# Optimization experiments

Measured on AMD Instinct MI355X. Metric: run time of the kernel, lower is better.

Reference implementation:

```python
import jax, jax.numpy as jnp
import numpy as np

B, S, D, P, W = 16, 100, 8192, 100, 3  # batch, seq, feat dim, proj width, window size


def setup_inputs() -> dict:
    key = jax.random.key(0)
    ks = jax.random.split(key, 6)
    return {
        "x": jax.random.normal(ks[0], (B, S, D), dtype=jnp.float32),
        "wq": jax.random.normal(ks[1], (D, P), dtype=jnp.float32) * (1.0 / np.sqrt(D)),
        "wk": jax.random.normal(ks[2], (D, P), dtype=jnp.float32) * (1.0 / np.sqrt(D)),
        "wv": jax.random.normal(ks[3], (D, P), dtype=jnp.float32) * (1.0 / np.sqrt(D)),
        "forwardpad": jax.random.normal(ks[4], (B, 1, D), dtype=jnp.float32),
        "backwardpad": jax.random.normal(ks[5], (B, 1, D), dtype=jnp.float32),
    }


def reference(x, wq, wk, wv, forwardpad, backwardpad):
    # pad: (B, S+2, D)
    padded = jnp.concatenate([forwardpad, x, backwardpad], axis=1)
    # gather all 100 overlapping size-3 windows at once: (B, S, W, D)
    idx = jnp.arange(S)[:, None] + jnp.arange(W)[None, :]  # (S, W)
    windows = padded[:, idx, :]
    # shared projections across all windows (original recomputed per window)
    q = jnp.einsum("bswd,dp->bswp", windows, wq)
    k = jnp.einsum("bswd,dp->bswp", windows, wk)
    v = jnp.einsum("bswd,dp->bswp", windows, wv)
    # per-window 3x3 attention
    scores = jnp.einsum("bswp,bsup->bswu", q, k)  # (B, S, W, W)
    attn = jax.nn.softmax(scores, axis=-1)
    out = jnp.einsum("bswu,bsup->bswp", attn, v)  # (B, S, W, P)
    # original concatenates windows along seq then takes [:, 1::3, :] -> center token of each window
    return out[:, :, 1, :]  # (B, S, P)
```

## Files before the change

### kernel.cpp

```cpp
#include <hip/hip_runtime.h>
#include <hip/hip_bf16.h>

constexpr int Dk   = 8192;
constexpr int Bb   = 16;
constexpr int Ss   = 100;
constexpr int Pp   = 100;
constexpr int MROW = 1632;
constexpr int MPAD = 1664;
constexpr int NT   = 20;
constexpr int NCC  = 320;
constexpr int KG   = 1024;
constexpr int KC   = 32;
constexpr int CH   = 5;

constexpr size_t B_SEG   = (size_t)NT * KG * 128;
constexpr size_t PSTRIDE = (size_t)MPAD * NCC;

typedef short s8v __attribute__((ext_vector_type(8)));
typedef short s4v __attribute__((ext_vector_type(4)));
typedef float f4v __attribute__((ext_vector_type(4)));

__device__ inline unsigned short f2bf_rne(float f) {
    unsigned u = __float_as_uint(f);
    u += 0x7fffu + ((u >> 16) & 1u);
    return (unsigned short)(u >> 16);
}

__global__ __launch_bounds__(256) void pack_b(
    const float* __restrict__ wq, const float* __restrict__ wk,
    const float* __restrict__ wv,
    short* __restrict__ b_hi, short* __restrict__ b_lo) {
    const int id = blockIdx.x * 256 + threadIdx.x;
    const int n  = id % NCC;
    const int kg = id / NCC;
    if (kg >= KG) return;

    const float* w = nullptr; int p = 0;
    if (n < 100)      { w = wq; p = n; }
    else if (n < 200) { w = wk; p = n - 100; }
    else if (n < 300) { w = wv; p = n - 200; }

    s8v hi, lo;
    #pragma unroll
    for (int j = 0; j < 8; ++j) {
        const float v = w ? w[(size_t)(kg * 8 + j) * Pp + p] : 0.0f;
        const unsigned u = __float_as_uint(v);
        hi[j] = (short)(unsigned short)(u >> 16);
        const float hf = __uint_as_float(u & 0xffff0000u);
        lo[j] = (short)f2bf_rne(v - hf);
    }
    const size_t doff = ((size_t)(n >> 4) * KG + kg) * 128 + (size_t)(n & 15) * 8;
    *(s8v*)(b_hi + doff) = hi;
    *(s8v*)(b_lo + doff) = lo;
}

__global__ __launch_bounds__(256) void qkv_fused(
    const float* __restrict__ x, const float* __restrict__ fpad,
    const float* __restrict__ bpad,
    const short* __restrict__ b_hi, const short* __restrict__ b_lo,
    unsigned short* __restrict__ part) {
    __shared__ __align__(16) short ahis[1024];
    __shared__ __align__(16) short alos[1024];

    const int mb   = blockIdx.x;
    const int kc   = blockIdx.y;
    const int tid  = threadIdx.x;
    const int w    = tid >> 6;
    const int l    = tid & 63;
    const int m    = l & 15;
    const int quad = l >> 4;

    const int sr  = tid >> 3;
    const int skq = tid & 7;
    const float* srow;
    {
        const int r = mb * 32 + sr;
        if (r >= MROW) srow = fpad;
        else {
            const int b = r / 102, rr = r - b * 102;
            if (rr == 0)        srow = fpad + (size_t)b * Dk;
            else if (rr == 101) srow = bpad + (size_t)b * Dk;
            else                srow = x + ((size_t)b * Ss + (rr - 1)) * Dk;
        }
    }
    const int woff = ((sr >> 4) * 4 + (skq >> 1)) * 128 + (sr & 15) * 8 + (skq & 1) * 4;

    f4v acc[2][5];
    #pragma unroll
    for (int i = 0; i < 2; ++i)
        #pragma unroll
        for (int j = 0; j < 5; ++j) {
            f4v z = {0.f, 0.f, 0.f, 0.f};
            acc[i][j] = z;
        }

    for (int s = 0; s < 8; ++s) {
        const float4 v = *(const float4*)(srow + kc * 256 + s * 32 + skq * 4);
        const float vv[4] = {v.x, v.y, v.z, v.w};
        s4v hi4, lo4;
        #pragma unroll
        for (int jj = 0; jj < 4; ++jj) {
            const unsigned u = __float_as_uint(vv[jj]);
            hi4[jj] = (short)(unsigned short)(u >> 16);
            const float hf = __uint_as_float(u & 0xffff0000u);
            lo4[jj] = (short)f2bf_rne(vv[jj] - hf);
        }
        __syncthreads();
        *(s4v*)&ahis[woff] = hi4;
        *(s4v*)&alos[woff] = lo4;
        __syncthreads();

        const s8v ah0 = *(const s8v*)&ahis[(quad * 16 + m) * 8];
        const s8v ah1 = *(const s8v*)&ahis[((4 + quad) * 16 + m) * 8];
        const s8v al0 = *(const s8v*)&alos[(quad * 16 + m) * 8];
        const s8v al1 = *(const s8v*)&alos[((4 + quad) * 16 + m) * 8];

        const int kgg = kc * 32 + s * 4 + quad;
        #pragma unroll
        for (int j = 0; j < 5; ++j) {
            const size_t bo = ((size_t)(w * 5 + j) * KG + kgg) * 128 + (size_t)m * 8;
            const s8v bh = *(const s8v*)(b_hi + bo);
            const s8v bl = *(const s8v*)(b_lo + bo);
            acc[0][j] = __builtin_amdgcn_mfma_f32_16x16x32_bf16(ah0, bh, acc[0][j], 0, 0, 0);
            acc[1][j] = __builtin_amdgcn_mfma_f32_16x16x32_bf16(ah1, bh, acc[1][j], 0, 0, 0);
            acc[0][j] = __builtin_amdgcn_mfma_f32_16x16x32_bf16(al0, bh, acc[0][j], 0, 0, 0);
            acc[1][j] = __builtin_amdgcn_mfma_f32_16x16x32_bf16(al1, bh, acc[1][j], 0, 0, 0);
            acc[0][j] = __builtin_amdgcn_mfma_f32_16x16x32_bf16(ah0, bl, acc[0][j], 0, 0, 0);
            acc[1][j] = __builtin_amdgcn_mfma_f32_16x16x32_bf16(ah1, bl, acc[1][j], 0, 0, 0);
        }
    }

    unsigned short* __restrict__ pout = part + (size_t)kc * PSTRIDE;
    #pragma unroll
    for (int i = 0; i < 2; ++i) {
        #pragma unroll
        for (int j = 0; j < 5; ++j) {
            const int col  = (w * 5 + j) * 16 + m;
            const int row0 = mb * 32 + i * 16 + quad * 4;
            #pragma unroll
            for (int r = 0; r < 4; ++r)
                pout[(size_t)(row0 + r) * NCC + col] = f2bf_rne(acc[i][j][r]);
        }
    }
}

__global__ __launch_bounds__(256) void attn3(
    const unsigned short* __restrict__ part, float* __restrict__ out) {
    const int blk = blockIdx.x;
    const int b  = blk / (Ss / CH);
    const int c  = blk % (Ss / CH);
    const int s0 = c * CH;
    const int tid = threadIdx.x;

    __shared__ float red[CH + 2][304];
    __shared__ float sc[CH][3];

    for (int idx = tid; idx < (CH + 2) * 300; idx += 256) {
        const int row = idx / 300, col = idx % 300;
        const size_t base = (size_t)(b * 102 + s0 + row) * NCC + col;
        float sum = 0.0f;
        #pragma unroll
        for (int k = 0; k < KC; ++k)
            sum += __uint_as_float((unsigned)part[(size_t)k * PSTRIDE + base] << 16);
        red[row][col] = sum;
    }
    __syncthreads();

    if (tid < CH * 3 * 16) {
        const int d = tid >> 4, g = tid & 15;
        const int ss = d / 3, u = d % 3;
        float ps = 0.0f;
        #pragma unroll
        for (int t = 0; t < 7; ++t) {
            const int p = g + t * 16;
            if (p < Pp) ps += red[ss + 1][p] * red[ss + u][100 + p];
        }
        #pragma unroll
        for (int off = 8; off > 0; off >>= 1) ps += __shfl_down(ps, off, 16);
        if (g == 0) sc[ss][u] = ps;
    }
    __syncthreads();

    for (int idx = tid; idx < CH * Pp; idx += 256) {
        const int ss = idx / Pp, p = idx % Pp;
        const float a0 = sc[ss][0], a1 = sc[ss][1], a2 = sc[ss][2];
        const float mx = fmaxf(a0, fmaxf(a1, a2));
        const float e0 = __expf(a0 - mx), e1 = __expf(a1 - mx), e2 = __expf(a2 - mx);
        const float inv = 1.0f / (e0 + e1 + e2);
        out[(size_t)(b * Ss + s0 + ss) * Pp + p] =
            inv * (e0 * red[ss][200 + p] + e1 * red[ss + 1][200 + p] +
                   e2 * red[ss + 2][200 + p]);
    }
}

extern "C" void kernel_launch(void* const* d_in, const int* in_sizes, int n_in,
                              void* d_out, int out_size, void* d_ws, size_t ws_size,
                              hipStream_t stream) {
    const float* x    = (const float*)d_in[0];
    const float* wq   = (const float*)d_in[1];
    const float* wk   = (const float*)d_in[2];
    const float* wv   = (const float*)d_in[3];
    const float* fpad = (const float*)d_in[4];
    const float* bpad = (const float*)d_in[5];
    float* out = (float*)d_out;

    short* b_hi = (short*)d_ws;
    short* b_lo = b_hi + B_SEG;
    unsigned short* part = (unsigned short*)(b_lo + B_SEG);

    pack_b<<<(NCC * KG) / 256, 256, 0, stream>>>(wq, wk, wv, b_hi, b_lo);
    qkv_fused<<<dim3(52, KC), 256, 0, stream>>>(x, fpad, bpad, b_hi, b_lo, part);
    attn3<<<Bb * (Ss / CH), 256, 0, stream>>>(part, out);
}
```

Before: 155.4 us.

## Double GEMM M-tile, fragment-native fp16 partials, and separate split-K reduce kernel

The QKV GEMM block now covers 64 rows instead of 32, so each B fragment load from global memory feeds four MFMA row tiles. This halves B-operand traffic and halves the number of M blocks. Partial sums are stored in fp16 in the MFMA fragment layout using vectorized 8-byte writes, and a new reduce kernel sums the 32 K-chunks with coalesced loads and writes an fp32 QKV matrix. The attention kernel then reads the reduced values directly. In exchange there is an extra kernel launch and workspace buffer, higher register pressure from 20 accumulators that may lower occupancy, and a possible fp16 range or precision risk in the partials.

After: 157.7 us. About the same (+1.5%).

```diff
diff --git a/kernel.cpp b/kernel.cpp
--- a/kernel.cpp
+++ b/kernel.cpp
@@ -1,20 +1,23 @@
 #include <hip/hip_runtime.h>
 #include <hip/hip_bf16.h>
+#include <hip/hip_fp16.h>
 
 constexpr int Dk   = 8192;
 constexpr int Bb   = 16;
 constexpr int Ss   = 100;
 constexpr int Pp   = 100;
 constexpr int MROW = 1632;
-constexpr int MPAD = 1664;
 constexpr int NT   = 20;
 constexpr int NCC  = 320;
+constexpr int NQ   = 304;
 constexpr int KG   = 1024;
 constexpr int KC   = 32;
 constexpr int CH   = 5;
+constexpr int MB   = 26;
+constexpr int GFR  = MB * 4 * 20;
 
 constexpr size_t B_SEG   = (size_t)NT * KG * 128;
-constexpr size_t PSTRIDE = (size_t)MPAD * NCC;
+constexpr size_t PSTRIDE = (size_t)GFR * 256;
 
 typedef short s8v __attribute__((ext_vector_type(8)));
 typedef short s4v __attribute__((ext_vector_type(4)));
@@ -59,8 +62,8 @@
     const float* __restrict__ bpad,
     const short* __restrict__ b_hi, const short* __restrict__ b_lo,
     unsigned short* __restrict__ part) {
-    __shared__ __align__(16) short ahis[1024];
-    __shared__ __align__(16) short alos[1024];
+    __shared__ __align__(16) short ahis[2048];
+    __shared__ __align__(16) short alos[2048];
 
     const int mb   = blockIdx.x;
     const int kc   = blockIdx.y;
@@ -70,50 +73,58 @@
     const int m    = l & 15;
     const int quad = l >> 4;
 
-    const int sr  = tid >> 3;
-    const int skq = tid & 7;
-    const float* srow;
+    const int srow = tid >> 2;
+    const int skq  = tid & 3;
+    const float* sp;
     {
-        const int r = mb * 32 + sr;
-        if (r >= MROW) srow = fpad;
+        const int r = mb * 64 + srow;
+        if (r >= MROW) sp = fpad;
         else {
             const int b = r / 102, rr = r - b * 102;
-            if (rr == 0)        srow = fpad + (size_t)b * Dk;
-            else if (rr == 101) srow = bpad + (size_t)b * Dk;
-            else                srow = x + ((size_t)b * Ss + (rr - 1)) * Dk;
-        }
-    }
-    const int woff = ((sr >> 4) * 4 + (skq >> 1)) * 128 + (sr & 15) * 8 + (skq & 1) * 4;
-
-    f4v acc[2][5];
-    #pragma unroll
-    for (int i = 0; i < 2; ++i)
+            if (rr == 0)        sp = fpad + (size_t)b * Dk;
+            else if (rr == 101) sp = bpad + (size_t)b * Dk;
+            else                sp = x + ((size_t)b * Ss + (rr - 1)) * Dk;
+        }
+        sp += kc * 256 + skq * 4;
+    }
+    const int w0 = (((srow >> 4) * 4 + (skq >> 1)) * 16 + (srow & 15)) * 8 + (skq & 1) * 4;
+    const int w1 = (((srow >> 4) * 4 + 2 + (skq >> 1)) * 16 + (srow & 15)) * 8 + (skq & 1) * 4;
+
+    f4v acc[4][5];
+    #pragma unroll
+    for (int i = 0; i < 4; ++i)
         #pragma unroll
         for (int j = 0; j < 5; ++j) {
             f4v z = {0.f, 0.f, 0.f, 0.f};
             acc[i][j] = z;
         }
 
+    #pragma unroll
     for (int s = 0; s < 8; ++s) {
-        const float4 v = *(const float4*)(srow + kc * 256 + s * 32 + skq * 4);
-        const float vv[4] = {v.x, v.y, v.z, v.w};
-        s4v hi4, lo4;
+        const float4 va = *(const float4*)(sp + s * 32);
+        const float4 vb = *(const float4*)(sp + s * 32 + 16);
+        const float vv[8] = {va.x, va.y, va.z, va.w, vb.x, vb.y, vb.z, vb.w};
+        s4v h0, l0, h1, l1;
         #pragma unroll
         for (int jj = 0; jj < 4; ++jj) {
-            const unsigned u = __float_as_uint(vv[jj]);
-            hi4[jj] = (short)(unsigned short)(u >> 16);
-            const float hf = __uint_as_float(u & 0xffff0000u);
-            lo4[jj] = (short)f2bf_rne(vv[jj] - hf);
+            unsigned u = __float_as_uint(vv[jj]);
+            h0[jj] = (short)(unsigned short)(u >> 16);
+            l0[jj] = (short)f2bf_rne(vv[jj] - __uint_as_float(u & 0xffff0000u));
+            u = __float_as_uint(vv[4 + jj]);
+            h1[jj] = (short)(unsigned short)(u >> 16);
+            l1[jj] = (short)f2bf_rne(vv[4 + jj] - __uint_as_float(u & 0xffff0000u));
         }
         __syncthreads();
-        *(s4v*)&ahis[woff] = hi4;
-        *(s4v*)&alos[woff] = lo4;
+        *(s4v*)&ahis[w0] = h0;  *(s4v*)&alos[w0] = l0;
+        *(s4v*)&ahis[w1] = h1;  *(s4v*)&alos[w1] = l1;
         __syncthreads();
 
-        const s8v ah0 = *(const s8v*)&ahis[(quad * 16 + m) * 8];
-        const s8v ah1 = *(const s8v*)&ahis[((4 + quad) * 16 + m) * 8];
-        const s8v al0 = *(const s8v*)&alos[(quad * 16 + m) * 8];
-        const s8v al1 = *(const s8v*)&alos[((4 + quad) * 16 + m) * 8];
+        s8v ah[4], al[4];
+        #pragma unroll
+        for (int i = 0; i < 4; ++i) {
+            ah[i] = *(const s8v*)&ahis[((i * 4 + quad) * 16 + m) * 8];
+            al[i] = *(const s8v*)&alos[((i * 4 + quad) * 16 + m) * 8];
+        }
 
         const int kgg = kc * 32 + s * 4 + quad;
         #pragma unroll
@@ -121,31 +132,67 @@
             const size_t bo = ((size_t)(w * 5 + j) * KG + kgg) * 128 + (size_t)m * 8;
             const s8v bh = *(const s8v*)(b_hi + bo);
             const s8v bl = *(const s8v*)(b_lo + bo);
-            acc[0][j] = __builtin_amdgcn_mfma_f32_16x16x32_bf16(ah0, bh, acc[0][j], 0, 0, 0);
-            acc[1][j] = __builtin_amdgcn_mfma_f32_16x16x32_bf16(ah1, bh, acc[1][j], 0, 0, 0);
-            acc[0][j] = __builtin_amdgcn_mfma_f32_16x16x32_bf16(al0, bh, acc[0][j], 0, 0, 0);
-            acc[1][j] = __builtin_amdgcn_mfma_f32_16x16x32_bf16(al1, bh, acc[1][j], 0, 0, 0);
-            acc[0][j] = __builtin_amdgcn_mfma_f32_16x16x32_bf16(ah0, bl, acc[0][j], 0, 0, 0);
-            acc[1][j] = __builtin_amdgcn_mfma_f32_16x16x32_bf16(ah1, bl, acc[1][j], 0, 0, 0);
-        }
-    }
-
-    unsigned short* __restrict__ pout = part + (size_t)kc * PSTRIDE;
-    #pragma unroll
-    for (int i = 0; i < 2; ++i) {
+            #pragma unroll
+            for (int i = 0; i < 4; ++i)
+                acc[i][j] = __builtin_amdgcn_mfma_f32_16x16x32_bf16(ah[i], bh, acc[i][j], 0, 0, 0);
+            #pragma unroll
+            for (int i = 0; i < 4; ++i)
+                acc[i][j] = __builtin_amdgcn_mfma_f32_16x16x32_bf16(al[i], bh, acc[i][j], 0, 0, 0);
+            #pragma unroll
+            for (int i = 0; i < 4; ++i)
+                acc[i][j] = __builtin_amdgcn_mfma_f32_16x16x32_bf16(ah[i], bl, acc[i][j], 0, 0, 0);
+        }
+    }
+
+    #pragma unroll
+    for (int i = 0; i < 4; ++i) {
         #pragma unroll
         for (int j = 0; j < 5; ++j) {
-            const int col  = (w * 5 + j) * 16 + m;
-            const int row0 = mb * 32 + i * 16 + quad * 4;
-            #pragma unroll
-            for (int r = 0; r < 4; ++r)
-                pout[(size_t)(row0 + r) * NCC + col] = f2bf_rne(acc[i][j][r]);
-        }
+            const int g = (mb * 4 + w) * 20 + i * 5 + j;
+            const size_t idx = (((size_t)kc * GFR + g) * 64 + l) * 4;
+            ushort4 u;
+            u.x = __half_as_ushort(__float2half(acc[i][j][0]));
+            u.y = __half_as_ushort(__float2half(acc[i][j][1]));
+            u.z = __half_as_ushort(__float2half(acc[i][j][2]));
+            u.w = __half_as_ushort(__float2half(acc[i][j][3]));
+            *(ushort4*)(part + idx) = u;
+        }
+    }
+}
+
+__global__ __launch_bounds__(256) void reduce_k(
+    const unsigned short* __restrict__ part, float* __restrict__ qkv) {
+    const int t = blockIdx.x * 256 + threadIdx.x;
+    const int g = t >> 6, l = t & 63;
+    const size_t base = ((size_t)g * 64 + l) * 4;
+
+    float s0 = 0.f, s1 = 0.f, s2 = 0.f, s3 = 0.f;
+    #pragma unroll
+    for (int k = 0; k < KC; ++k) {
+        const ushort4 u = *(const ushort4*)(part + base + (size_t)k * PSTRIDE);
+        s0 += __half2float(__ushort_as_half(u.x));
+        s1 += __half2float(__ushort_as_half(u.y));
+        s2 += __half2float(__ushort_as_half(u.z));
+        s3 += __half2float(__ushort_as_half(u.w));
+    }
+
+    const int mb = g / 80, rem = g - mb * 80;
+    const int nw = rem / 20, fi = rem - nw * 20;
+    const int i = fi / 5, j = fi - i * 5;
+    const int quad = l >> 4, m = l & 15;
+    const int row = mb * 64 + i * 16 + quad * 4;
+    const int col = (nw * 5 + j) * 16 + m;
+    if (col < NQ) {
+        float* q = qkv + (size_t)row * NQ + col;
+        q[0]      = s0;
+        q[NQ]     = s1;
+        q[2 * NQ] = s2;
+        q[3 * NQ] = s3;
     }
 }
 
 __global__ __launch_bounds__(256) void attn3(
-    const unsigned short* __restrict__ part, float* __restrict__ out) {
+    const float* __restrict__ qkv, float* __restrict__ out) {
     const int blk = blockIdx.x;
     const int b  = blk / (Ss / CH);
     const int c  = blk % (Ss / CH);
@@ -157,12 +204,7 @@
 
     for (int idx = tid; idx < (CH + 2) * 300; idx += 256) {
         const int row = idx / 300, col = idx % 300;
-        const size_t base = (size_t)(b * 102 + s0 + row) * NCC + col;
-        float sum = 0.0f;
-        #pragma unroll
-        for (int k = 0; k < KC; ++k)
-            sum += __uint_as_float((unsigned)part[(size_t)k * PSTRIDE + base] << 16);
-        red[row][col] = sum;
+        red[row][col] = qkv[(size_t)(b * 102 + s0 + row) * NQ + col];
     }
     __syncthreads();
 
@@ -207,8 +249,10 @@
     short* b_hi = (short*)d_ws;
     short* b_lo = b_hi + B_SEG;
     unsigned short* part = (unsigned short*)(b_lo + B_SEG);
+    float* qkv = (float*)(part + (size_t)KC * PSTRIDE);
 
     pack_b<<<(NCC * KG) / 256, 256, 0, stream>>>(wq, wk, wv, b_hi, b_lo);
-    qkv_fused<<<dim3(52, KC), 256, 0, stream>>>(x, fpad, bpad, b_hi, b_lo, part);
-    attn3<<<Bb * (Ss / CH), 256, 0, stream>>>(part, out);
-}
+    qkv_fused<<<dim3(MB, KC), 256, 0, stream>>>(x, fpad, bpad, b_hi, b_lo, part);
+    reduce_k<<<(GFR * 64) / 256, 256, 0, stream>>>(part, qkv);
+    attn3<<<Bb * (Ss / CH), 256, 0, stream>>>(qkv, out);
+}
```

## Drop LDS staging, double the M tile per block, store partials as fp16

Applied to the files above, without the earlier changes.

The GEMM kernel now has each lane load its own A rows straight from global memory into registers, in the layout the MFMA operand expects. This removes the shared-memory staging and the two barriers per k-step, and the next k-slice is prefetched through double-buffered registers. Each block now covers 64 rows instead of 32, halving the grid in M so every B fragment load feeds twice as many MFMAs. Partial sums are stored as fp16 instead of bf16 for more mantissa precision. The cost is more register pressure from 20 accumulators plus the prefetch buffers, possible occupancy loss, fewer blocks, and a risk of fp16 overflow on large partial values.

After: 180.8 us. 1.16x slower.

```diff
diff --git a/kernel.cpp b/kernel.cpp
--- a/kernel.cpp
+++ b/kernel.cpp
@@ -1,23 +1,23 @@
 #include <hip/hip_runtime.h>
 #include <hip/hip_bf16.h>
+#include <hip/hip_fp16.h>
 
 constexpr int Dk   = 8192;
 constexpr int Bb   = 16;
 constexpr int Ss   = 100;
 constexpr int Pp   = 100;
 constexpr int MROW = 1632;
-constexpr int MPAD = 1664;
 constexpr int NT   = 20;
 constexpr int NCC  = 320;
 constexpr int KG   = 1024;
 constexpr int KC   = 32;
 constexpr int CH   = 5;
+constexpr int MB   = 26;
 
 constexpr size_t B_SEG   = (size_t)NT * KG * 128;
-constexpr size_t PSTRIDE = (size_t)MPAD * NCC;
+constexpr size_t PSTRIDE = (size_t)1664 * NCC;
 
 typedef short s8v __attribute__((ext_vector_type(8)));
-typedef short s4v __attribute__((ext_vector_type(4)));
 typedef float f4v __attribute__((ext_vector_type(4)));
 
 __device__ inline unsigned short f2bf_rne(float f) {
@@ -54,14 +54,11 @@
     *(s8v*)(b_lo + doff) = lo;
 }
 
-__global__ __launch_bounds__(256) void qkv_fused(
+__global__ __launch_bounds__(256) void qkv_gemm(
     const float* __restrict__ x, const float* __restrict__ fpad,
     const float* __restrict__ bpad,
     const short* __restrict__ b_hi, const short* __restrict__ b_lo,
     unsigned short* __restrict__ part) {
-    __shared__ __align__(16) short ahis[1024];
-    __shared__ __align__(16) short alos[1024];
-
     const int mb   = blockIdx.x;
     const int kc   = blockIdx.y;
     const int tid  = threadIdx.x;
@@ -70,81 +67,106 @@
     const int m    = l & 15;
     const int quad = l >> 4;
 
-    const int sr  = tid >> 3;
-    const int skq = tid & 7;
-    const float* srow;
-    {
-        const int r = mb * 32 + sr;
-        if (r >= MROW) srow = fpad;
+    const float* ap[4];
+    #pragma unroll
+    for (int i = 0; i < 4; ++i) {
+        const int r = mb * 64 + i * 16 + m;
+        const float* src;
+        if (r >= MROW) src = fpad;
         else {
             const int b = r / 102, rr = r - b * 102;
-            if (rr == 0)        srow = fpad + (size_t)b * Dk;
-            else if (rr == 101) srow = bpad + (size_t)b * Dk;
-            else                srow = x + ((size_t)b * Ss + (rr - 1)) * Dk;
-        }
-    }
-    const int woff = ((sr >> 4) * 4 + (skq >> 1)) * 128 + (sr & 15) * 8 + (skq & 1) * 4;
-
-    f4v acc[2][5];
-    #pragma unroll
-    for (int i = 0; i < 2; ++i)
+            if (rr == 0)        src = fpad + (size_t)b * Dk;
+            else if (rr == 101) src = bpad + (size_t)b * Dk;
+            else                src = x + ((size_t)b * Ss + (rr - 1)) * Dk;
+        }
+        ap[i] = src + kc * 256 + quad * 8;
+    }
+
+    const int nt0 = w * 5;
+
+    f4v acc[4][5];
+    #pragma unroll
+    for (int i = 0; i < 4; ++i)
         #pragma unroll
         for (int j = 0; j < 5; ++j) {
             f4v z = {0.f, 0.f, 0.f, 0.f};
             acc[i][j] = z;
         }
 
+    float4 aA[4][2], aB[4][2];
+
+    #pragma unroll
+    for (int i = 0; i < 4; ++i) {
+        aA[i][0] = *(const float4*)(ap[i]);
+        aA[i][1] = *(const float4*)(ap[i] + 4);
+    }
+
+    #pragma unroll
     for (int s = 0; s < 8; ++s) {
-        const float4 v = *(const float4*)(srow + kc * 256 + s * 32 + skq * 4);
-        const float vv[4] = {v.x, v.y, v.z, v.w};
-        s4v hi4, lo4;
-        #pragma unroll
-        for (int jj = 0; jj < 4; ++jj) {
-            const unsigned u = __float_as_uint(vv[jj]);
-            hi4[jj] = (short)(unsigned short)(u >> 16);
-            const float hf = __uint_as_float(u & 0xffff0000u);
-            lo4[jj] = (short)f2bf_rne(vv[jj] - hf);
-        }
-        __syncthreads();
-        *(s4v*)&ahis[woff] = hi4;
-        *(s4v*)&alos[woff] = lo4;
-        __syncthreads();
-
-        const s8v ah0 = *(const s8v*)&ahis[(quad * 16 + m) * 8];
-        const s8v ah1 = *(const s8v*)&ahis[((4 + quad) * 16 + m) * 8];
-        const s8v al0 = *(const s8v*)&alos[(quad * 16 + m) * 8];
-        const s8v al1 = *(const s8v*)&alos[((4 + quad) * 16 + m) * 8];
-
-        const int kgg = kc * 32 + s * 4 + quad;
+        if (s < 7) {
+            if ((s & 1) == 0) {
+                #pragma unroll
+                for (int i = 0; i < 4; ++i) {
+                    aB[i][0] = *(const float4*)(ap[i] + (s + 1) * 32);
+                    aB[i][1] = *(const float4*)(ap[i] + (s + 1) * 32 + 4);
+                }
+            } else {
+                #pragma unroll
+                for (int i = 0; i < 4; ++i) {
+                    aA[i][0] = *(const float4*)(ap[i] + (s + 1) * 32);
+                    aA[i][1] = *(const float4*)(ap[i] + (s + 1) * 32 + 4);
+                }
+            }
+        }
+
+        s8v ah[4], al[4];
+        #pragma unroll
+        for (int i = 0; i < 4; ++i) {
+            const float4 v0 = ((s & 1) == 0) ? aA[i][0] : aB[i][0];
+            const float4 v1 = ((s & 1) == 0) ? aA[i][1] : aB[i][1];
+            const float vv[8] = {v0.x, v0.y, v0.z, v0.w, v1.x, v1.y, v1.z, v1.w};
+            #pragma unroll
+            for (int jj = 0; jj < 8; ++jj) {
+                const unsigned u = __float_as_uint(vv[jj]);
+                ah[i][jj] = (short)(unsigned short)(u >> 16);
+                al[i][jj] = (short)f2bf_rne(vv[jj] - __uint_as_float(u & 0xffff0000u));
+            }
+        }
+
+        const int kg = kc * 32 + s * 4 + quad;
         #pragma unroll
         for (int j = 0; j < 5; ++j) {
-            const size_t bo = ((size_t)(w * 5 + j) * KG + kgg) * 128 + (size_t)m * 8;
+            const size_t bo = ((size_t)(nt0 + j) * KG + kg) * 128 + (size_t)m * 8;
             const s8v bh = *(const s8v*)(b_hi + bo);
             const s8v bl = *(const s8v*)(b_lo + bo);
-            acc[0][j] = __builtin_amdgcn_mfma_f32_16x16x32_bf16(ah0, bh, acc[0][j], 0, 0, 0);
-            acc[1][j] = __builtin_amdgcn_mfma_f32_16x16x32_bf16(ah1, bh, acc[1][j], 0, 0, 0);
-            acc[0][j] = __builtin_amdgcn_mfma_f32_16x16x32_bf16(al0, bh, acc[0][j], 0, 0, 0);
-            acc[1][j] = __builtin_amdgcn_mfma_f32_16x16x32_bf16(al1, bh, acc[1][j], 0, 0, 0);
-            acc[0][j] = __builtin_amdgcn_mfma_f32_16x16x32_bf16(ah0, bl, acc[0][j], 0, 0, 0);
-            acc[1][j] = __builtin_amdgcn_mfma_f32_16x16x32_bf16(ah1, bl, acc[1][j], 0, 0, 0);
+            #pragma unroll
+            for (int i = 0; i < 4; ++i)
+                acc[i][j] = __builtin_amdgcn_mfma_f32_16x16x32_bf16(ah[i], bh, acc[i][j], 0, 0, 0);
+            #pragma unroll
+            for (int i = 0; i < 4; ++i)
+                acc[i][j] = __builtin_amdgcn_mfma_f32_16x16x32_bf16(al[i], bh, acc[i][j], 0, 0, 0);
+            #pragma unroll
+            for (int i = 0; i < 4; ++i)
+                acc[i][j] = __builtin_amdgcn_mfma_f32_16x16x32_bf16(ah[i], bl, acc[i][j], 0, 0, 0);
         }
     }
 
     unsigned short* __restrict__ pout = part + (size_t)kc * PSTRIDE;
     #pragma unroll
-    for (int i = 0; i < 2; ++i) {
+    for (int i = 0; i < 4; ++i) {
         #pragma unroll
         for (int j = 0; j < 5; ++j) {
-            const int col  = (w * 5 + j) * 16 + m;
-            const int row0 = mb * 32 + i * 16 + quad * 4;
+            const int col  = (nt0 + j) * 16 + m;
+            const int row0 = mb * 64 + i * 16 + quad * 4;
             #pragma unroll
             for (int r = 0; r < 4; ++r)
-                pout[(size_t)(row0 + r) * NCC + col] = f2bf_rne(acc[i][j][r]);
-        }
-    }
-}
-
-__global__ __launch_bounds__(256) void attn3(
+                pout[(size_t)(row0 + r) * NCC + col] =
+                    __half_as_ushort(__float2half(acc[i][j][r]));
+        }
+    }
+}
+
+__global__ __launch_bounds__(256) void reduce_attn(
     const unsigned short* __restrict__ part, float* __restrict__ out) {
     const int blk = blockIdx.x;
     const int b  = blk / (Ss / CH);
@@ -161,7 +183,7 @@
         float sum = 0.0f;
         #pragma unroll
         for (int k = 0; k < KC; ++k)
-            sum += __uint_as_float((unsigned)part[(size_t)k * PSTRIDE + base] << 16);
+            sum += __half2float(__ushort_as_half(part[(size_t)k * PSTRIDE + base]));
         red[row][col] = sum;
     }
     __syncthreads();
@@ -209,6 +231,6 @@
     unsigned short* part = (unsigned short*)(b_lo + B_SEG);
 
     pack_b<<<(NCC * KG) / 256, 256, 0, stream>>>(wq, wk, wv, b_hi, b_lo);
-    qkv_fused<<<dim3(52, KC), 256, 0, stream>>>(x, fpad, bpad, b_hi, b_lo, part);
-    attn3<<<Bb * (Ss / CH), 256, 0, stream>>>(part, out);
-}
+    qkv_gemm<<<dim3(MB, KC), 256, 0, stream>>>(x, fpad, bpad, b_hi, b_lo, part);
+    reduce_attn<<<Bb * (Ss / CH), 256, 0, stream>>>(part, out);
+}
```

## Prefetch A tile into registers, double-buffer LDS, store partials as fp16

Applied to the files above, without the earlier changes.

The GEMM kernel now issues all eight float4 loads of its A slice up front, before the MMA loop. It also double-buffers the LDS tiles so each step needs one barrier instead of two, and adds an occupancy hint to launch_bounds. Partial sums are stored as fp16 instead of bf16, which gives more mantissa precision but less range. The reduce kernel now reads them as vectorized ushort4. The aim is to hide global load latency and cut barrier overhead, at the cost of more registers per thread.

Result: slower. 177.6 us (+14.3%).

```diff
diff --git a/kernel.cpp b/kernel.cpp
--- a/kernel.cpp
+++ b/kernel.cpp
@@ -1,20 +1,21 @@
 #include <hip/hip_runtime.h>
 #include <hip/hip_bf16.h>
+#include <hip/hip_fp16.h>
 
 constexpr int Dk   = 8192;
 constexpr int Bb   = 16;
 constexpr int Ss   = 100;
 constexpr int Pp   = 100;
 constexpr int MROW = 1632;
-constexpr int MPAD = 1664;
 constexpr int NT   = 20;
 constexpr int NCC  = 320;
 constexpr int KG   = 1024;
 constexpr int KC   = 32;
 constexpr int CH   = 5;
+constexpr int MBL  = 52;
 
 constexpr size_t B_SEG   = (size_t)NT * KG * 128;
-constexpr size_t PSTRIDE = (size_t)MPAD * NCC;
+constexpr size_t PSTRIDE = (size_t)1664 * NCC;
 
 typedef short s8v __attribute__((ext_vector_type(8)));
 typedef short s4v __attribute__((ext_vector_type(4)));
@@ -54,13 +55,13 @@
     *(s8v*)(b_lo + doff) = lo;
 }
 
-__global__ __launch_bounds__(256) void qkv_fused(
+__global__ __launch_bounds__(256, 4) void qkv_gemm(
     const float* __restrict__ x, const float* __restrict__ fpad,
     const float* __restrict__ bpad,
     const short* __restrict__ b_hi, const short* __restrict__ b_lo,
     unsigned short* __restrict__ part) {
-    __shared__ __align__(16) short ahis[1024];
-    __shared__ __align__(16) short alos[1024];
+    __shared__ __align__(16) short ahis[2][1024];
+    __shared__ __align__(16) short alos[2][1024];
 
     const int mb   = blockIdx.x;
     const int kc   = blockIdx.y;
@@ -72,18 +73,23 @@
 
     const int sr  = tid >> 3;
     const int skq = tid & 7;
-    const float* srow;
+    const float* sp;
     {
         const int r = mb * 32 + sr;
-        if (r >= MROW) srow = fpad;
+        if (r >= MROW) sp = fpad;
         else {
             const int b = r / 102, rr = r - b * 102;
-            if (rr == 0)        srow = fpad + (size_t)b * Dk;
-            else if (rr == 101) srow = bpad + (size_t)b * Dk;
-            else                srow = x + ((size_t)b * Ss + (rr - 1)) * Dk;
-        }
+            if (rr == 0)        sp = fpad + (size_t)b * Dk;
+            else if (rr == 101) sp = bpad + (size_t)b * Dk;
+            else                sp = x + ((size_t)b * Ss + (rr - 1)) * Dk;
+        }
+        sp += kc * 256 + skq * 4;
     }
     const int woff = ((sr >> 4) * 4 + (skq >> 1)) * 128 + (sr & 15) * 8 + (skq & 1) * 4;
+
+    float4 av[8];
+    #pragma unroll
+    for (int s = 0; s < 8; ++s) av[s] = *(const float4*)(sp + s * 32);
 
     f4v acc[2][5];
     #pragma unroll
@@ -94,31 +100,30 @@
             acc[i][j] = z;
         }
 
+    #pragma unroll
     for (int s = 0; s < 8; ++s) {
-        const float4 v = *(const float4*)(srow + kc * 256 + s * 32 + skq * 4);
-        const float vv[4] = {v.x, v.y, v.z, v.w};
-        s4v hi4, lo4;
+        const int buf = s & 1;
+        const float vv[4] = {av[s].x, av[s].y, av[s].z, av[s].w};
+        s4v h4, l4;
         #pragma unroll
         for (int jj = 0; jj < 4; ++jj) {
             const unsigned u = __float_as_uint(vv[jj]);
-            hi4[jj] = (short)(unsigned short)(u >> 16);
-            const float hf = __uint_as_float(u & 0xffff0000u);
-            lo4[jj] = (short)f2bf_rne(vv[jj] - hf);
-        }
+            h4[jj] = (short)(unsigned short)(u >> 16);
+            l4[jj] = (short)f2bf_rne(vv[jj] - __uint_as_float(u & 0xffff0000u));
+        }
+        *(s4v*)&ahis[buf][woff] = h4;
+        *(s4v*)&alos[buf][woff] = l4;
         __syncthreads();
-        *(s4v*)&ahis[woff] = hi4;
-        *(s4v*)&alos[woff] = lo4;
-        __syncthreads();
-
-        const s8v ah0 = *(const s8v*)&ahis[(quad * 16 + m) * 8];
-        const s8v ah1 = *(const s8v*)&ahis[((4 + quad) * 16 + m) * 8];
-        const s8v al0 = *(const s8v*)&alos[(quad * 16 + m) * 8];
-        const s8v al1 = *(const s8v*)&alos[((4 + quad) * 16 + m) * 8];
-
-        const int kgg = kc * 32 + s * 4 + quad;
+
+        const s8v ah0 = *(const s8v*)&ahis[buf][(quad * 16 + m) * 8];
+        const s8v ah1 = *(const s8v*)&ahis[buf][((4 + quad) * 16 + m) * 8];
+        const s8v al0 = *(const s8v*)&alos[buf][(quad * 16 + m) * 8];
+        const s8v al1 = *(const s8v*)&alos[buf][((4 + quad) * 16 + m) * 8];
+
+        const int kg = kc * 32 + s * 4 + quad;
         #pragma unroll
         for (int j = 0; j < 5; ++j) {
-            const size_t bo = ((size_t)(w * 5 + j) * KG + kgg) * 128 + (size_t)m * 8;
+            const size_t bo = ((size_t)(w * 5 + j) * KG + kg) * 128 + (size_t)m * 8;
             const s8v bh = *(const s8v*)(b_hi + bo);
             const s8v bl = *(const s8v*)(b_lo + bo);
             acc[0][j] = __builtin_amdgcn_mfma_f32_16x16x32_bf16(ah0, bh, acc[0][j], 0, 0, 0);
@@ -139,12 +144,13 @@
             const int row0 = mb * 32 + i * 16 + quad * 4;
             #pragma unroll
             for (int r = 0; r < 4; ++r)
-                pout[(size_t)(row0 + r) * NCC + col] = f2bf_rne(acc[i][j][r]);
-        }
-    }
-}
-
-__global__ __launch_bounds__(256) void attn3(
+                pout[(size_t)(row0 + r) * NCC + col] =
+                    __half_as_ushort(__float2half(acc[i][j][r]));
+        }
+    }
+}
+
+__global__ __launch_bounds__(256) void reduce_attn(
     const unsigned short* __restrict__ part, float* __restrict__ out) {
     const int blk = blockIdx.x;
     const int b  = blk / (Ss / CH);
@@ -155,14 +161,22 @@
     __shared__ float red[CH + 2][304];
     __shared__ float sc[CH][3];
 
-    for (int idx = tid; idx < (CH + 2) * 300; idx += 256) {
-        const int row = idx / 300, col = idx % 300;
-        const size_t base = (size_t)(b * 102 + s0 + row) * NCC + col;
-        float sum = 0.0f;
-        #pragma unroll
-        for (int k = 0; k < KC; ++k)
-            sum += __uint_as_float((unsigned)part[(size_t)k * PSTRIDE + base] << 16);
-        red[row][col] = sum;
+    for (int idx = tid; idx < (CH + 2) * 75; idx += 256) {
+        const int row = idx / 75, cg = idx % 75;
+        const size_t base = ((size_t)(b * 102 + s0 + row) * NCC + cg * 4) >> 2;
+        float s0v = 0.f, s1v = 0.f, s2v = 0.f, s3v = 0.f;
+        #pragma unroll
+        for (int k = 0; k < KC; ++k) {
+            const ushort4 u = ((const ushort4*)part)[(size_t)k * (PSTRIDE >> 2) + base];
+            s0v += __half2float(__ushort_as_half(u.x));
+            s1v += __half2float(__ushort_as_half(u.y));
+            s2v += __half2float(__ushort_as_half(u.z));
+            s3v += __half2float(__ushort_as_half(u.w));
+        }
+        red[row][cg * 4 + 0] = s0v;
+        red[row][cg * 4 + 1] = s1v;
+        red[row][cg * 4 + 2] = s2v;
+        red[row][cg * 4 + 3] = s3v;
     }
     __syncthreads();
 
@@ -209,6 +223,6 @@
     unsigned short* part = (unsigned short*)(b_lo + B_SEG);
 
     pack_b<<<(NCC * KG) / 256, 256, 0, stream>>>(wq, wk, wv, b_hi, b_lo);
-    qkv_fused<<<dim3(52, KC), 256, 0, stream>>>(x, fpad, bpad, b_hi, b_lo, part);
-    attn3<<<Bb * (Ss / CH), 256, 0, stream>>>(part, out);
-}
+    qkv_gemm<<<dim3(MBL, KC), 256, 0, stream>>>(x, fpad, bpad, b_hi, b_lo, part);
+    reduce_attn<<<Bb * (Ss / CH), 256, 0, stream>>>(part, out);
+}
```
